# Kernel optimization log

Hardware: AMD Instinct MI355X
Metric: run time of the kernel (lower is better)

Reference implementation:

```python
import jax, jax.numpy as jnp
import numpy as np

B, L, D = 8, 1024, 1024
H = 16
DPH = D // H  # 64
MAX_REL = 32  # relative position clip; vocab = 2*MAX_REL+1 (use_neg_dist=True)


def setup_inputs() -> dict:
    key = jax.random.key(0)
    ks = jax.random.split(key, 12)
    s = 1.0 / np.sqrt(D)
    return {
        "key": jax.random.normal(ks[0], (B, L, D), jnp.float32),
        "value": jax.random.normal(ks[1], (B, L, D), jnp.float32),
        "query": jax.random.normal(ks[2], (B, L, D), jnp.float32),
        "Wq": jax.random.normal(ks[3], (D, D), jnp.float32) * s,
        "bq": jnp.zeros((D,), jnp.float32),
        "Wk": jax.random.normal(ks[4], (D, D), jnp.float32) * s,
        "bk": jnp.zeros((D,), jnp.float32),
        "Wv": jax.random.normal(ks[5], (D, D), jnp.float32) * s,
        "bv": jnp.zeros((D,), jnp.float32),
        "Wo": jax.random.normal(ks[6], (D, D), jnp.float32) * s,
        "bo": jnp.zeros((D,), jnp.float32),
        "rel_emb": jax.random.normal(ks[7], (2 * MAX_REL + 1, DPH), jnp.float32) * 0.02,
    }


def reference(key, value, query, Wq, bq, Wk, bk, Wv, bv, Wo, bo, rel_emb):
    # shape: [B, L, D] -> [B, H, L, DPH]
    def shape(x):
        return x.reshape(B, L, H, DPH).transpose(0, 2, 1, 3)

    q = shape(query @ Wq.T + bq) / np.float32(np.sqrt(DPH))
    k = shape(key @ Wk.T + bk)
    v = shape(value @ Wv.T + bv)

    # relative position indices, clipped to [-MAX_REL, MAX_REL], shifted to [0, 2*MAX_REL]
    r = jnp.arange(L)
    dist = jnp.clip(r[None, :] - r[:, None], -MAX_REL, MAX_REL) + MAX_REL  # [L, L]
    rel = rel_emb[dist]  # [L, L, DPH]; same table for keys and values

    # scores = QK^T + Q . rel_keys  (relative_matmul with transpose=True)
    scores = jnp.einsum('bhqd,bhkd->bhqk', q, k) + jnp.einsum('bhqd,qkd->bhqk', q, rel)
    attn = jax.nn.softmax(scores.astype(jnp.float32), axis=-1).astype(q.dtype)

    # context = attn @ V + attn . rel_values (relative_matmul with transpose=False)
    ctx = jnp.einsum('bhqk,bhkd->bhqd', attn, v) + jnp.einsum('bhqk,qkd->bhqd', attn, rel)
    ctx = ctx.transpose(0, 2, 1, 3).reshape(B, L, D)
    out = ctx @ Wo.T + bo
    return out, attn
```

## Files before the change

### kernel.cpp

```cpp
#include <hip/hip_runtime.h>

typedef unsigned short u16;
typedef _Float16 f16;
typedef __attribute__((ext_vector_type(8))) _Float16 f16x8;
typedef __attribute__((ext_vector_type(4))) _Float16 f16x4;
typedef __attribute__((ext_vector_type(2))) _Float16 f16x2;
typedef __attribute__((ext_vector_type(4))) float f32x4;

#define MFMA16(acc, a, b) acc = __builtin_amdgcn_mfma_f32_16x16x32_f16(a, b, acc, 0, 0, 0)

__device__ __forceinline__ void gl2lds16(const void* g, void* l) {
  __builtin_amdgcn_global_load_lds(
      (const __attribute__((address_space(1))) void*)g,
      (__attribute__((address_space(3))) void*)l, 16, 0, 0);
}

__global__ __launch_bounds__(256) void cvt_f32_f16_k(const float* __restrict__ src, f16* __restrict__ dst,
                                                     int n8) {
  int i = blockIdx.x * 256 + threadIdx.x;
  if (i >= n8) return;
  const float* p = src + (size_t)i * 8;
  f32x4 a = *(const f32x4*)p;
  f32x4 b = *(const f32x4*)(p + 4);
  f16x8 o;
#pragma unroll
  for (int j = 0; j < 4; j++) {
    o[j] = (f16)a[j];
    o[j + 4] = (f16)b[j];
  }
  *(f16x8*)(dst + (size_t)i * 8) = o;
}

template <int EPI>
__global__ __launch_bounds__(256) void gemm_bt(const f16* __restrict__ A, const f16* __restrict__ Wt,
                                               const float* __restrict__ bias, void* __restrict__ outv,
                                               int M, int N, int K, float scale) {
  const int nbn = N >> 7;
  int id = blockIdx.x;
  int m0 = (id / nbn) << 7;
  int n0 = (id % nbn) << 7;
  int tid = threadIdx.x;
  int w = tid >> 6, lane = tid & 63, c = lane & 15, g = lane >> 4;
  int wm = (w >> 1) << 6, wn = (w & 1) << 6;

  __shared__ f16 As[128 * 32];
  __shared__ f16 Bs[128 * 32];

  f32x4 acc[4][4] = {};
  int ci0 = tid, ci1 = tid + 256;

  for (int k0 = 0; k0 < K; k0 += 32) {
    __syncthreads();
    gl2lds16(A + (size_t)(m0 + (ci0 >> 2)) * K + k0 + ((ci0 & 3) << 3), As + w * 512);
    gl2lds16(A + (size_t)(m0 + (ci1 >> 2)) * K + k0 + ((ci1 & 3) << 3), As + w * 512 + 2048);
    gl2lds16(Wt + (size_t)(n0 + (ci0 >> 2)) * K + k0 + ((ci0 & 3) << 3), Bs + w * 512);
    gl2lds16(Wt + (size_t)(n0 + (ci1 >> 2)) * K + k0 + ((ci1 & 3) << 3), Bs + w * 512 + 2048);
    __syncthreads();
    f16x8 af[4], bf[4];
#pragma unroll
    for (int mf = 0; mf < 4; mf++) af[mf] = *(const f16x8*)(As + ((wm + mf * 16 + c) << 5) + (g << 3));
#pragma unroll
    for (int nf = 0; nf < 4; nf++) bf[nf] = *(const f16x8*)(Bs + ((wn + nf * 16 + c) << 5) + (g << 3));
#pragma unroll
    for (int mf = 0; mf < 4; mf++)
#pragma unroll
      for (int nf = 0; nf < 4; nf++) MFMA16(acc[mf][nf], af[mf], bf[nf]);
  }

#pragma unroll
  for (int mf = 0; mf < 4; mf++)
#pragma unroll
    for (int nf = 0; nf < 4; nf++) {
      if (EPI == 2) {
        int row0 = m0 + wm + mf * 16 + (g << 2);
        int col = n0 + wn + nf * 16 + c;
        f16x4 vv;
#pragma unroll
        for (int r = 0; r < 4; r++) vv[r] = (f16)((acc[mf][nf][r] + bias[col]) * scale);
        size_t idx = (size_t)((row0 >> 10) * 16 + (col >> 6)) * 65536 + (size_t)(col & 63) * 1024 + (row0 & 1023);
        *(f16x4*)((f16*)outv + idx) = vv;
      } else {
#pragma unroll
        for (int r = 0; r < 4; r++) {
          int row = m0 + wm + mf * 16 + (g << 2) + r;
          int col = n0 + wn + nf * 16 + c;
          float v = (acc[mf][nf][r] + bias[col]) * scale;
          if (EPI == 0) {
            ((float*)outv)[(size_t)row * N + col] = v;
          } else {
            size_t idx = (size_t)((row >> 10) * 16 + (col >> 6)) * 65536 + ((row & 1023) << 6) + (col & 63);
            ((f16*)outv)[idx] = (f16)v;
          }
        }
      }
    }
}

__global__ __launch_bounds__(256) void attn_fused(const f16* __restrict__ Q, const f16* __restrict__ Km,
                                                  const f16* __restrict__ Vt, const f16* __restrict__ rel,
                                                  float* __restrict__ attn, f16* __restrict__ ctx) {
  int id = blockIdx.x;
  int sw = ((id & 7) << 10) + (id >> 3);
  int bh = sw >> 6;
  int q0 = (sw & 63) << 4;
  int b = bh >> 4, h = bh & 15;
  int tid = threadIdx.x;
  int w = tid >> 6, lane = tid & 63, c = lane & 15, g = lane >> 4;

  __shared__ float qrel_s[16 * 68];
  __shared__ float rmax[4][16], rsum[4][16], rlo[4][16], rhi[4][16];
  __shared__ float lo_s[16], hi_s[16];
  __shared__ f16 P_lds[1024 * 18];
  __shared__ f16 rel_s[65 * 64];

  const f16* Qb = Q + ((size_t)bh << 16);
  const f16* Kb = Km + ((size_t)bh << 16);
  const f16* Vtb = Vt + ((size_t)bh << 16);

  for (int i = tid; i < 65 * 64; i += 256) rel_s[i] = rel[i];

  f16x8 aq0 = *(const f16x8*)(Qb + ((q0 + c) << 6) + (g << 3));
  f16x8 aq1 = *(const f16x8*)(Qb + ((q0 + c) << 6) + 32 + (g << 3));

  if (w == 0) {
#pragma unroll
    for (int tf = 0; tf < 5; tf++) {
      int t = tf * 16 + c;
      int tc = (t < 65) ? t : 0;
      f32x4 ar = {};
      f16x8 b0 = *(const f16x8*)(rel + (tc << 6) + (g << 3));
      f16x8 b1 = *(const f16x8*)(rel + (tc << 6) + 32 + (g << 3));
      MFMA16(ar, aq0, b0);
      MFMA16(ar, aq1, b1);
      if (t < 65) {
#pragma unroll
        for (int r = 0; r < 4; r++) qrel_s[((g << 2) + r) * 68 + t] = ar[r];
      }
    }
  }
  __syncthreads();

  float s[16][4];
  int kbase = w << 8;
#pragma unroll
  for (int f = 0; f < 16; f++) {
    int kcol = kbase + (f << 4) + c;
    f32x4 a4 = {};
    f16x8 b0 = *(const f16x8*)(Kb + (kcol << 6) + (g << 3));
    f16x8 b1 = *(const f16x8*)(Kb + (kcol << 6) + 32 + (g << 3));
    MFMA16(a4, aq0, b0);
    MFMA16(a4, aq1, b1);
#pragma unroll
    for (int r = 0; r < 4; r++) {
      int rowl = (g << 2) + r;
      int d = kcol - (q0 + rowl);
      int t = (d < -32 ? -32 : (d > 32 ? 32 : d)) + 32;
      s[f][r] = a4[r] + qrel_s[rowl * 68 + t];
    }
  }

  float m[4] = {-3.0e38f, -3.0e38f, -3.0e38f, -3.0e38f};
#pragma unroll
  for (int f = 0; f < 16; f++)
#pragma unroll
    for (int r = 0; r < 4; r++) m[r] = fmaxf(m[r], s[f][r]);
#pragma unroll
  for (int mk = 1; mk <= 8; mk <<= 1)
#pragma unroll
    for (int r = 0; r < 4; r++) m[r] = fmaxf(m[r], __shfl_xor(m[r], mk, 64));
  if (c == 0) {
#pragma unroll
    for (int r = 0; r < 4; r++) rmax[w][(g << 2) + r] = m[r];
  }
  __syncthreads();
  float gm[4];
#pragma unroll
  for (int r = 0; r < 4; r++) {
    int rowl = (g << 2) + r;
    gm[r] = fmaxf(fmaxf(rmax[0][rowl], rmax[1][rowl]), fmaxf(rmax[2][rowl], rmax[3][rowl]));
  }
  float sum[4] = {0, 0, 0, 0}, lo[4] = {0, 0, 0, 0}, hi[4] = {0, 0, 0, 0};
#pragma unroll
  for (int f = 0; f < 16; f++)
#pragma unroll
    for (int r = 0; r < 4; r++) {
      float p = __expf(s[f][r] - gm[r]);
      s[f][r] = p;
      sum[r] += p;
      int d = (kbase + (f << 4) + c) - (q0 + (g << 2) + r);
      if (d <= -32) lo[r] += p;
      if (d >= 32) hi[r] += p;
    }
#pragma unroll
  for (int mk = 1; mk <= 8; mk <<= 1)
#pragma unroll
    for (int r = 0; r < 4; r++) {
      sum[r] += __shfl_xor(sum[r], mk, 64);
      lo[r] += __shfl_xor(lo[r], mk, 64);
      hi[r] += __shfl_xor(hi[r], mk, 64);
    }
  if (c == 0) {
#pragma unroll
    for (int r = 0; r < 4; r++) {
      int rowl = (g << 2) + r;
      rsum[w][rowl] = sum[r];
      rlo[w][rowl] = lo[r];
      rhi[w][rowl] = hi[r];
    }
  }
  __syncthreads();
  float inv[4];
#pragma unroll
  for (int r = 0; r < 4; r++) {
    int rowl = (g << 2) + r;
    float tot = rsum[0][rowl] + rsum[1][rowl] + rsum[2][rowl] + rsum[3][rowl];
    inv[r] = 1.0f / tot;
  }
  if (w == 0 && c == 0) {
#pragma unroll
    for (int r = 0; r < 4; r++) {
      int rowl = (g << 2) + r;
      float l4 = rlo[0][rowl] + rlo[1][rowl] + rlo[2][rowl] + rlo[3][rowl];
      float h4 = rhi[0][rowl] + rhi[1][rowl] + rhi[2][rowl] + rhi[3][rowl];
      lo_s[rowl] = l4 * inv[r];
      hi_s[rowl] = h4 * inv[r];
    }
  }

  float* ab = attn + ((size_t)bh << 20);
#pragma unroll
  for (int f = 0; f < 16; f++) {
    int k = kbase + (f << 4) + c;
    f16 ph[4];
#pragma unroll
    for (int r = 0; r < 4; r++) {
      float p = s[f][r] * inv[r];
      ab[((size_t)(q0 + (g << 2) + r) << 10) | (size_t)k] = p;
      ph[r] = (f16)p;
    }
    int koff = k * 18 + (g << 2);
    f16x2 p01 = {ph[0], ph[1]};
    f16x2 p23 = {ph[2], ph[3]};
    *(f16x2*)(P_lds + koff) = p01;
    *(f16x2*)(P_lds + koff + 2) = p23;
  }
  __syncthreads();

  f32x4 pv0 = {}, pv1 = {};
  const f16* vrow = Vtb + (size_t)((w << 4) + c) * 1024;
#pragma unroll 4
  for (int kk = 0; kk < 1024; kk += 64) {
    f16x8 aV0 = *(const f16x8*)(vrow + kk + (g << 3));
    f16x8 bP0;
#pragma unroll
    for (int j = 0; j < 8; j++) bP0[j] = P_lds[(kk + (g << 3) + j) * 18 + c];
    MFMA16(pv0, aV0, bP0);
    f16x8 aV1 = *(const f16x8*)(vrow + kk + 32 + (g << 3));
    f16x8 bP1;
#pragma unroll
    for (int j = 0; j < 8; j++) bP1[j] = P_lds[(kk + 32 + (g << 3) + j) * 18 + c];
    MFMA16(pv1, aV1, bP1);
  }

  int qg = q0 + c;
  float cval[4];
#pragma unroll
  for (int r = 0; r < 4; r++) {
    int d = (w << 4) + (g << 2) + r;
    cval[r] = pv0[r] + pv1[r] + lo_s[c] * (float)rel_s[d] + hi_s[c] * (float)rel_s[64 * 64 + d];
  }
  for (int t = 1; t < 64; t++) {
    int k = qg + t - 32;
    if (k >= 0 && k < 1024) {
      float pk = (float)P_lds[k * 18 + c];
#pragma unroll
      for (int r = 0; r < 4; r++) {
        int d = (w << 4) + (g << 2) + r;
        cval[r] += pk * (float)rel_s[t * 64 + d];
      }
    }
  }

#pragma unroll
  for (int r = 0; r < 4; r++) {
    int d = (w << 4) + (g << 2) + r;
    ctx[(((size_t)(b << 10) + qg) << 10) + (h << 6) + d] = (f16)cval[r];
  }
}

extern "C" void kernel_launch(void* const* d_in, const int* in_sizes, int n_in, void* d_out, int out_size,
                              void* d_ws, size_t ws_size, hipStream_t stream) {
  const float* key = (const float*)d_in[0];
  const float* value = (const float*)d_in[1];
  const float* query = (const float*)d_in[2];
  const float* Wq = (const float*)d_in[3];
  const float* bq = (const float*)d_in[4];
  const float* Wk = (const float*)d_in[5];
  const float* bk = (const float*)d_in[6];
  const float* Wv = (const float*)d_in[7];
  const float* bv = (const float*)d_in[8];
  const float* Wo = (const float*)d_in[9];
  const float* bo = (const float*)d_in[10];
  const float* rel = (const float*)d_in[11];

  char* ws = (char*)d_ws;
  f16* Xf = (f16*)(ws);
  f16* Qw = (f16*)(ws + (16u << 20));
  f16* Kw = (f16*)(ws + (32u << 20));
  f16* Vw = (f16*)(ws + (48u << 20));
  f16* Wf = (f16*)(ws + (64u << 20));
  f16* relf = (f16*)(ws + (66u << 20));

  float* outp = (float*)d_out;
  float* attnp = outp + (size_t)8 * 1024 * 1024;

  dim3 blk(256);
  const int n8x = (8 * 1024 * 1024) / 8;
  const int n8w = (1024 * 1024) / 8;
  const int n8r = (65 * 64) / 8;

  cvt_f32_f16_k<<<(n8r + 255) / 256, blk, 0, stream>>>(rel, relf, n8r);

  cvt_f32_f16_k<<<n8w / 256, blk, 0, stream>>>(Wq, Wf, n8w);
  cvt_f32_f16_k<<<n8x / 256, blk, 0, stream>>>(query, Xf, n8x);
  gemm_bt<1><<<512, blk, 0, stream>>>(Xf, Wf, bq, Qw, 8192, 1024, 1024, 0.125f);

  cvt_f32_f16_k<<<n8w / 256, blk, 0, stream>>>(Wk, Wf, n8w);
  cvt_f32_f16_k<<<n8x / 256, blk, 0, stream>>>(key, Xf, n8x);
  gemm_bt<1><<<512, blk, 0, stream>>>(Xf, Wf, bk, Kw, 8192, 1024, 1024, 1.0f);

  cvt_f32_f16_k<<<n8w / 256, blk, 0, stream>>>(Wv, Wf, n8w);
  cvt_f32_f16_k<<<n8x / 256, blk, 0, stream>>>(value, Xf, n8x);
  gemm_bt<2><<<512, blk, 0, stream>>>(Xf, Wf, bv, Vw, 8192, 1024, 1024, 1.0f);

  attn_fused<<<8192, blk, 0, stream>>>(Qw, Kw, Vw, relf, attnp, Xf);

  cvt_f32_f16_k<<<n8w / 256, blk, 0, stream>>>(Wo, Wf, n8w);
  gemm_bt<0><<<512, blk, 0, stream>>>(Xf, Wf, bo, outp, 8192, 1024, 1024, 1.0f);
}
```

Baseline: 507.3 us.

## Fuse input f32→f16 conversion into batched QKV GEMM and merge weight conversions

The separate activation conversion kernels are removed: the QKV GEMM now loads fp32 activations directly, converts them in registers and writes f16 tiles to LDS. The three projections run in a single 1536-block launch. All weight and rel-table conversions are merged into one kernel, which cuts launch count and the 16MB f16 round trips per input. In exchange, the A-tile load now goes through registers instead of async global-to-LDS, and it reads twice the bytes per tile inside the GEMM loop.

```diff
diff --git a/kernel.cpp b/kernel.cpp
--- a/kernel.cpp
+++ b/kernel.cpp
@@ -15,10 +15,7 @@
       (__attribute__((address_space(3))) void*)l, 16, 0, 0);
 }
 
-__global__ __launch_bounds__(256) void cvt_f32_f16_k(const float* __restrict__ src, f16* __restrict__ dst,
-                                                     int n8) {
-  int i = blockIdx.x * 256 + threadIdx.x;
-  if (i >= n8) return;
+__device__ __forceinline__ void cvt8(const float* __restrict__ src, f16* __restrict__ dst, int i) {
   const float* p = src + (size_t)i * 8;
   f32x4 a = *(const f32x4*)p;
   f32x4 b = *(const f32x4*)(p + 4);
@@ -31,14 +28,37 @@
   *(f16x8*)(dst + (size_t)i * 8) = o;
 }
 
-template <int EPI>
-__global__ __launch_bounds__(256) void gemm_bt(const f16* __restrict__ A, const f16* __restrict__ Wt,
-                                               const float* __restrict__ bias, void* __restrict__ outv,
-                                               int M, int N, int K, float scale) {
-  const int nbn = N >> 7;
+__global__ __launch_bounds__(256) void cvt_all(const float* __restrict__ Wq, const float* __restrict__ Wk,
+                                               const float* __restrict__ Wv, const float* __restrict__ Wo,
+                                               const float* __restrict__ rel, f16* __restrict__ f0,
+                                               f16* __restrict__ f1, f16* __restrict__ f2,
+                                               f16* __restrict__ f3, f16* __restrict__ fr) {
+  const int NW = 131072;
+  int i = blockIdx.x * 256 + threadIdx.x;
+  if (i < NW) cvt8(Wq, f0, i);
+  else if (i < 2 * NW) cvt8(Wk, f1, i - NW);
+  else if (i < 3 * NW) cvt8(Wv, f2, i - 2 * NW);
+  else if (i < 4 * NW) cvt8(Wo, f3, i - 3 * NW);
+  else if (i < 4 * NW + 520) cvt8(rel, fr, i - 4 * NW);
+}
+
+__global__ __launch_bounds__(256) void gemm_qkv(const float* __restrict__ Aq, const float* __restrict__ Ak,
+                                                const float* __restrict__ Av, const f16* __restrict__ W0,
+                                                const f16* __restrict__ W1, const f16* __restrict__ W2,
+                                                const float* __restrict__ b0, const float* __restrict__ b1,
+                                                const float* __restrict__ b2, f16* __restrict__ O0,
+                                                f16* __restrict__ O1, f16* __restrict__ O2) {
   int id = blockIdx.x;
-  int m0 = (id / nbn) << 7;
-  int n0 = (id % nbn) << 7;
+  int which = id >> 9;
+  int iid = id & 511;
+  const float* A = (which == 0) ? Aq : (which == 1) ? Ak : Av;
+  const f16* Wt = (which == 0) ? W0 : (which == 1) ? W1 : W2;
+  const float* bias = (which == 0) ? b0 : (which == 1) ? b1 : b2;
+  f16* out = (which == 0) ? O0 : (which == 1) ? O1 : O2;
+  float scale = (which == 0) ? 0.125f : 1.0f;
+
+  int m0 = (iid >> 3) << 7;
+  int n0 = (iid & 7) << 7;
   int tid = threadIdx.x;
   int w = tid >> 6, lane = tid & 63, c = lane & 15, g = lane >> 4;
   int wm = (w >> 1) << 6, wn = (w & 1) << 6;
@@ -48,13 +68,29 @@
 
   f32x4 acc[4][4] = {};
   int ci0 = tid, ci1 = tid + 256;
-
-  for (int k0 = 0; k0 < K; k0 += 32) {
+  int r0 = ci0 >> 2, ks0 = (ci0 & 3) << 3;
+  int r1 = ci1 >> 2, ks1 = (ci1 & 3) << 3;
+
+  for (int k0 = 0; k0 < 1024; k0 += 32) {
     __syncthreads();
-    gl2lds16(A + (size_t)(m0 + (ci0 >> 2)) * K + k0 + ((ci0 & 3) << 3), As + w * 512);
-    gl2lds16(A + (size_t)(m0 + (ci1 >> 2)) * K + k0 + ((ci1 & 3) << 3), As + w * 512 + 2048);
-    gl2lds16(Wt + (size_t)(n0 + (ci0 >> 2)) * K + k0 + ((ci0 & 3) << 3), Bs + w * 512);
-    gl2lds16(Wt + (size_t)(n0 + (ci1 >> 2)) * K + k0 + ((ci1 & 3) << 3), Bs + w * 512 + 2048);
+    gl2lds16(Wt + (size_t)(n0 + (ci0 >> 2)) * 1024 + k0 + ((ci0 & 3) << 3), Bs + w * 512);
+    gl2lds16(Wt + (size_t)(n0 + (ci1 >> 2)) * 1024 + k0 + ((ci1 & 3) << 3), Bs + w * 512 + 2048);
+    {
+      const float* ap0 = A + (size_t)(m0 + r0) * 1024 + k0 + ks0;
+      const float* ap1 = A + (size_t)(m0 + r1) * 1024 + k0 + ks1;
+      f32x4 x0 = *(const f32x4*)ap0, x1 = *(const f32x4*)(ap0 + 4);
+      f32x4 y0 = *(const f32x4*)ap1, y1 = *(const f32x4*)(ap1 + 4);
+      f16x8 h0, h1;
+#pragma unroll
+      for (int j = 0; j < 4; j++) {
+        h0[j] = (f16)x0[j];
+        h0[j + 4] = (f16)x1[j];
+        h1[j] = (f16)y0[j];
+        h1[j + 4] = (f16)y1[j];
+      }
+      *(f16x8*)(As + (r0 << 5) + ks0) = h0;
+      *(f16x8*)(As + (r1 << 5) + ks1) = h1;
+    }
     __syncthreads();
     f16x8 af[4], bf[4];
 #pragma unroll
@@ -71,29 +107,68 @@
   for (int mf = 0; mf < 4; mf++)
 #pragma unroll
     for (int nf = 0; nf < 4; nf++) {
-      if (EPI == 2) {
-        int row0 = m0 + wm + mf * 16 + (g << 2);
-        int col = n0 + wn + nf * 16 + c;
+      int row0 = m0 + wm + mf * 16 + (g << 2);
+      int col = n0 + wn + nf * 16 + c;
+      if (which == 2) {
         f16x4 vv;
 #pragma unroll
-        for (int r = 0; r < 4; r++) vv[r] = (f16)((acc[mf][nf][r] + bias[col]) * scale);
+        for (int r = 0; r < 4; r++) vv[r] = (f16)(acc[mf][nf][r] + bias[col]);
         size_t idx = (size_t)((row0 >> 10) * 16 + (col >> 6)) * 65536 + (size_t)(col & 63) * 1024 + (row0 & 1023);
-        *(f16x4*)((f16*)outv + idx) = vv;
+        *(f16x4*)(out + idx) = vv;
       } else {
 #pragma unroll
         for (int r = 0; r < 4; r++) {
-          int row = m0 + wm + mf * 16 + (g << 2) + r;
-          int col = n0 + wn + nf * 16 + c;
-          float v = (acc[mf][nf][r] + bias[col]) * scale;
-          if (EPI == 0) {
-            ((float*)outv)[(size_t)row * N + col] = v;
-          } else {
-            size_t idx = (size_t)((row >> 10) * 16 + (col >> 6)) * 65536 + ((row & 1023) << 6) + (col & 63);
-            ((f16*)outv)[idx] = (f16)v;
-          }
+          int row = row0 + r;
+          size_t idx = (size_t)((row >> 10) * 16 + (col >> 6)) * 65536 + ((row & 1023) << 6) + (col & 63);
+          out[idx] = (f16)((acc[mf][nf][r] + bias[col]) * scale);
         }
       }
     }
+}
+
+__global__ __launch_bounds__(256) void gemm_out(const f16* __restrict__ A, const f16* __restrict__ Wt,
+                                                const float* __restrict__ bias, float* __restrict__ out) {
+  int id = blockIdx.x;
+  int m0 = (id >> 3) << 7;
+  int n0 = (id & 7) << 7;
+  int tid = threadIdx.x;
+  int w = tid >> 6, lane = tid & 63, c = lane & 15, g = lane >> 4;
+  int wm = (w >> 1) << 6, wn = (w & 1) << 6;
+
+  __shared__ f16 As[128 * 32];
+  __shared__ f16 Bs[128 * 32];
+
+  f32x4 acc[4][4] = {};
+  int ci0 = tid, ci1 = tid + 256;
+
+  for (int k0 = 0; k0 < 1024; k0 += 32) {
+    __syncthreads();
+    gl2lds16(A + (size_t)(m0 + (ci0 >> 2)) * 1024 + k0 + ((ci0 & 3) << 3), As + w * 512);
+    gl2lds16(A + (size_t)(m0 + (ci1 >> 2)) * 1024 + k0 + ((ci1 & 3) << 3), As + w * 512 + 2048);
+    gl2lds16(Wt + (size_t)(n0 + (ci0 >> 2)) * 1024 + k0 + ((ci0 & 3) << 3), Bs + w * 512);
+    gl2lds16(Wt + (size_t)(n0 + (ci1 >> 2)) * 1024 + k0 + ((ci1 & 3) << 3), Bs + w * 512 + 2048);
+    __syncthreads();
+    f16x8 af[4], bf[4];
+#pragma unroll
+    for (int mf = 0; mf < 4; mf++) af[mf] = *(const f16x8*)(As + ((wm + mf * 16 + c) << 5) + (g << 3));
+#pragma unroll
+    for (int nf = 0; nf < 4; nf++) bf[nf] = *(const f16x8*)(Bs + ((wn + nf * 16 + c) << 5) + (g << 3));
+#pragma unroll
+    for (int mf = 0; mf < 4; mf++)
+#pragma unroll
+      for (int nf = 0; nf < 4; nf++) MFMA16(acc[mf][nf], af[mf], bf[nf]);
+  }
+
+#pragma unroll
+  for (int mf = 0; mf < 4; mf++)
+#pragma unroll
+    for (int nf = 0; nf < 4; nf++)
+#pragma unroll
+      for (int r = 0; r < 4; r++) {
+        int row = m0 + wm + mf * 16 + (g << 2) + r;
+        int col = n0 + wn + nf * 16 + c;
+        out[(size_t)row * 1024 + col] = acc[mf][nf][r] + bias[col];
+      }
 }
 
 __global__ __launch_bounds__(256) void attn_fused(const f16* __restrict__ Q, const f16* __restrict__ Km,
@@ -304,37 +379,22 @@
   const float* rel = (const float*)d_in[11];
 
   char* ws = (char*)d_ws;
-  f16* Xf = (f16*)(ws);
+  f16* ctx = (f16*)(ws);
+  f16* Wf0 = (f16*)(ws);
+  f16* Wf1 = (f16*)(ws + (2u << 20));
+  f16* Wf2 = (f16*)(ws + (4u << 20));
   f16* Qw = (f16*)(ws + (16u << 20));
   f16* Kw = (f16*)(ws + (32u << 20));
   f16* Vw = (f16*)(ws + (48u << 20));
-  f16* Wf = (f16*)(ws + (64u << 20));
+  f16* Wf3 = (f16*)(ws + (64u << 20));
   f16* relf = (f16*)(ws + (66u << 20));
 
   float* outp = (float*)d_out;
   float* attnp = outp + (size_t)8 * 1024 * 1024;
 
   dim3 blk(256);
-  const int n8x = (8 * 1024 * 1024) / 8;
-  const int n8w = (1024 * 1024) / 8;
-  const int n8r = (65 * 64) / 8;
-
-  cvt_f32_f16_k<<<(n8r + 255) / 256, blk, 0, stream>>>(rel, relf, n8r);
-
-  cvt_f32_f16_k<<<n8w / 256, blk, 0, stream>>>(Wq, Wf, n8w);
-  cvt_f32_f16_k<<<n8x / 256, blk, 0, stream>>>(query, Xf, n8x);
-  gemm_bt<1><<<512, blk, 0, stream>>>(Xf, Wf, bq, Qw, 8192, 1024, 1024, 0.125f);
-
-  cvt_f32_f16_k<<<n8w / 256, blk, 0, stream>>>(Wk, Wf, n8w);
-  cvt_f32_f16_k<<<n8x / 256, blk, 0, stream>>>(key, Xf, n8x);
-  gemm_bt<1><<<512, blk, 0, stream>>>(Xf, Wf, bk, Kw, 8192, 1024, 1024, 1.0f);
-
-  cvt_f32_f16_k<<<n8w / 256, blk, 0, stream>>>(Wv, Wf, n8w);
-  cvt_f32_f16_k<<<n8x / 256, blk, 0, stream>>>(value, Xf, n8x);
-  gemm_bt<2><<<512, blk, 0, stream>>>(Xf, Wf, bv, Vw, 8192, 1024, 1024, 1.0f);
-
-  attn_fused<<<8192, blk, 0, stream>>>(Qw, Kw, Vw, relf, attnp, Xf);
-
-  cvt_f32_f16_k<<<n8w / 256, blk, 0, stream>>>(Wo, Wf, n8w);
-  gemm_bt<0><<<512, blk, 0, stream>>>(Xf, Wf, bo, outp, 8192, 1024, 1024, 1.0f);
-}
+  cvt_all<<<2051, blk, 0, stream>>>(Wq, Wk, Wv, Wo, rel, Wf0, Wf1, Wf2, Wf3, relf);
+  gemm_qkv<<<1536, blk, 0, stream>>>(query, key, value, Wf0, Wf1, Wf2, bq, bk, bv, Qw, Kw, Vw);
+  attn_fused<<<8192, blk, 0, stream>>>(Qw, Kw, Vw, relf, attnp, ctx);
+  gemm_out<<<512, blk, 0, stream>>>(ctx, Wf3, bo, outp);
+}
```

Measured after the change: 499.1 us. No clear change (-1.6%).
